# Performance work log

Hardware: AMD Instinct MI355X
Metric: run time of the kernel (lower is better)

## Reference

```python
import jax, jax.numpy as jnp
import numpy as np

N_NODES = 100000
N_EDGES = 1600000
K = 5  # TAGConv hops
F_IN, F_HID, F_OUT = 64, 128, 64


def setup_inputs() -> dict:
    key = jax.random.key(0)
    ks = jax.random.split(key, 6)
    x = jax.random.normal(ks[0], (N_NODES, F_IN), dtype=jnp.float32)
    edge_index = jax.random.randint(ks[1], (2, N_EDGES), 0, N_NODES, dtype=jnp.int32)
    edge_weight = jax.random.uniform(ks[2], (N_EDGES,), dtype=jnp.float32)
    # TAGConv layer l has (K+1) weight matrices stacked as [K+1, in, out] + one bias
    W0 = jax.random.normal(ks[3], (K + 1, F_IN, F_HID), dtype=jnp.float32) * 0.05
    b0 = jnp.zeros((F_HID,), dtype=jnp.float32)
    W1 = jax.random.normal(ks[4], (K + 1, F_HID, F_OUT), dtype=jnp.float32) * 0.05
    b1 = jnp.zeros((F_OUT,), dtype=jnp.float32)
    return {"x": x, "edge_index": edge_index, "edge_weight": edge_weight,
            "W0": W0, "b0": b0, "W1": W1, "b1": b1}


def _gcn_norm(edge_weight, row, col):
    # symmetric normalization, no added self-loops (TAGConv default with edge_weight)
    deg = jax.ops.segment_sum(edge_weight, col, num_segments=N_NODES)
    safe_deg = jnp.where(deg > 0, deg, 1.0)
    dis = jnp.where(deg > 0, jax.lax.rsqrt(safe_deg), 0.0)  # deg^-1/2, 0 for isolated
    return dis[row] * edge_weight * dis[col]


def _tag_conv(x, row, col, norm, W, b):
    # out = sum_{k=0..K} (A_norm^k x) @ W[k] + b
    out = x @ W[0]
    h = x
    for k in range(1, K + 1):
        msg = h[row] * norm[:, None]                    # gather + scale  [E, F]
        h = jax.ops.segment_sum(msg, col, num_segments=N_NODES)  # scatter-add [N, F]
        out = out + h @ W[k]
    return out + b


def reference(x, edge_index, edge_weight, W0, b0, W1, b1):
    row, col = edge_index[0], edge_index[1]
    norm = _gcn_norm(edge_weight, row, col)
    h = jax.nn.leaky_relu(_tag_conv(x, row, col, norm, W0, b0), negative_slope=0.01)
    h = jax.nn.leaky_relu(_tag_conv(h, row, col, norm, W1, b1), negative_slope=0.01)
    return h
```

## Files before the change

### kernel.cpp

```cpp
#include <hip/hip_runtime.h>


namespace {
constexpr int NN = 100000;
constexpr int NE = 1600000;
constexpr int TPB = 256;

typedef __attribute__((ext_vector_type(8))) short short8v;
typedef __attribute__((ext_vector_type(4))) float float4v;

__device__ __forceinline__ float bflo(unsigned p) { return __uint_as_float(p << 16); }
__device__ __forceinline__ float bfhi(unsigned p) { return __uint_as_float(p & 0xffff0000u); }
__device__ __forceinline__ unsigned f2bf(float x) {
  unsigned u = __float_as_uint(x);
  return (u + 0x7fffu + ((u >> 16) & 1u)) >> 16;
}
__device__ __forceinline__ unsigned pack2(float lo, float hi) {
  return f2bf(lo) | (f2bf(hi) << 16);
}

__global__ void pass1_kernel(const int* __restrict__ col, const float* __restrict__ w,
                             unsigned long long* __restrict__ acc64, int* __restrict__ rank) {
  int e = blockIdx.x * TPB + threadIdx.x;
  if (e >= NE) return;
  int c = col[e];
  unsigned long long v = (1ULL << 40) | (unsigned long long)__float2uint_rn(w[e] * 16777216.0f);
  unsigned long long old = atomicAdd(&acc64[c], v);
  rank[e] = (int)(old >> 40);
}

__global__ void dis_kernel(const unsigned long long* __restrict__ acc64,
                           float* __restrict__ dis) {
  int n = blockIdx.x * TPB + threadIdx.x;
  if (n >= NN) return;
  unsigned long long u = acc64[n] & ((1ULL << 40) - 1);
  float d = (float)u * (1.0f / 16777216.0f);
  dis[n] = d > 0.f ? rsqrtf(d) : 0.f;
}

__global__ void scan1_kernel(const unsigned long long* __restrict__ acc64,
                             int* __restrict__ excl, int* __restrict__ btot) {
  __shared__ int sh[1024];
  int i = blockIdx.x * 1024 + threadIdx.x;
  int v = (i < NN) ? (int)(acc64[i] >> 40) : 0;
  sh[threadIdx.x] = v;
  __syncthreads();
  for (int ofs = 1; ofs < 1024; ofs <<= 1) {
    int t = (threadIdx.x >= ofs) ? sh[threadIdx.x - ofs] : 0;
    __syncthreads();
    sh[threadIdx.x] += t;
    __syncthreads();
  }
  if (i < NN) excl[i] = sh[threadIdx.x] - v;
  if (threadIdx.x == 1023) btot[blockIdx.x] = sh[1023];
}

__global__ void scan2_kernel(int* __restrict__ btot, int nb) {
  __shared__ int sh[128];
  int t = threadIdx.x;
  if (t < nb) sh[t] = btot[t];
  __syncthreads();
  if (t == 0) {
    int run = 0;
    for (int b = 0; b < nb; ++b) { int x = sh[b]; sh[b] = run; run += x; }
  }
  __syncthreads();
  if (t < nb) btot[t] = sh[t];
}

__global__ void scan3_kernel(const int* __restrict__ excl, const int* __restrict__ btot,
                             int* __restrict__ rowptr) {
  int i = blockIdx.x * TPB + threadIdx.x;
  if (i < NN) rowptr[i] = excl[i] + btot[i >> 10];
  if (i == NN) rowptr[NN] = NE;
}

__global__ void fill2_kernel(const int* __restrict__ row, const int* __restrict__ col,
                             const float* __restrict__ w, const float* __restrict__ dis,
                             const int* __restrict__ rank, const int* __restrict__ rowptr,
                             int2* __restrict__ edges) {
  int e = blockIdx.x * TPB + threadIdx.x;
  if (e >= NE) return;
  int r = row[e], c = col[e];
  float nw = dis[r] * w[e] * dis[c];
  edges[rowptr[c] + rank[e]] = make_int2(r, __float_as_int(nw));
}

__global__ void wfrag0_kernel(const float* __restrict__ W0, short* __restrict__ F) {
  int t = blockIdx.x * TPB + threadIdx.x;
  if (t >= 12 * 8 * 64) return;
  int l = t & 63, nt = (t >> 6) & 7, s = t >> 9;
  int c = nt * 16 + (l & 15);
  int kb = s * 32 + (l >> 4) * 8;
  short8v v;
#pragma unroll
  for (int j = 0; j < 8; ++j) v[j] = (short)f2bf(W0[(kb + j) * 128 + c]);
  *(short8v*)(F + (size_t)t * 8) = v;
}

__global__ void wfrag1_kernel(const float* __restrict__ W1, short* __restrict__ F) {
  int t = blockIdx.x * TPB + threadIdx.x;
  if (t >= 4 * 24 * 64) return;
  int l = t & 63, nt = (t >> 6) % 24, s = t / (64 * 24);
  int J = nt * 16 + (l & 15);
  int fb = s * 32 + (l >> 4) * 8;
  const float* Wb = W1 + (size_t)(J >> 6) * (128 * 64) + (J & 63);
  short8v v;
#pragma unroll
  for (int j = 0; j < 8; ++j) v[j] = (short)f2bf(Wb[(size_t)(fb + j) * 64]);
  *(short8v*)(F + (size_t)t * 8) = v;
}

__global__ void convx_kernel(const float* __restrict__ x, unsigned* __restrict__ hcat) {
  unsigned idx = blockIdx.x * (unsigned)TPB + threadIdx.x;
  if (idx >= (unsigned)NN * 32u) return;
  unsigned n = idx >> 5, p = idx & 31u;
  float2 v = *(const float2*)(x + (size_t)n * 64 + p * 2);
  hcat[(size_t)n * 192 + p] = pack2(v.x, v.y);
}

__device__ __forceinline__ void fma8(float* a, uint4 p, float w) {
  a[0] = fmaf(bflo(p.x), w, a[0]); a[1] = fmaf(bfhi(p.x), w, a[1]);
  a[2] = fmaf(bflo(p.y), w, a[2]); a[3] = fmaf(bfhi(p.y), w, a[3]);
  a[4] = fmaf(bflo(p.z), w, a[4]); a[5] = fmaf(bfhi(p.z), w, a[5]);
  a[6] = fmaf(bflo(p.w), w, a[6]); a[7] = fmaf(bfhi(p.w), w, a[7]);
}

template <bool YADD, bool FINAL>
__global__ void hop_kernel(const unsigned short* __restrict__ src, int sstride,
                           const int2* __restrict__ edges, const int* __restrict__ rowptr,
                           const unsigned short* __restrict__ y,
                           unsigned short* __restrict__ dst, int dstride,
                           const float* __restrict__ bias, float* __restrict__ outf) {
  unsigned n = blockIdx.x * 32u + (threadIdx.x >> 3);
  unsigned lane = threadIdx.x & 7u;
  unsigned f0 = lane * 8u;
  int e = rowptr[n], e1 = rowptr[n + 1];
  float a[8] = {};
  for (; e + 1 < e1; e += 2) {
    int2 d0 = edges[e], d1 = edges[e + 1];
    uint4 p0 = *(const uint4*)(src + (size_t)(unsigned)d0.x * sstride + f0);
    uint4 p1 = *(const uint4*)(src + (size_t)(unsigned)d1.x * sstride + f0);
    fma8(a, p0, __int_as_float(d0.y));
    fma8(a, p1, __int_as_float(d1.y));
  }
  if (e < e1) {
    int2 d0 = edges[e];
    uint4 p0 = *(const uint4*)(src + (size_t)(unsigned)d0.x * sstride + f0);
    fma8(a, p0, __int_as_float(d0.y));
  }
  if (YADD) {
    uint4 yv = *(const uint4*)(y + (size_t)n * 384 + f0);
    a[0] += bflo(yv.x); a[1] += bfhi(yv.x);
    a[2] += bflo(yv.y); a[3] += bfhi(yv.y);
    a[4] += bflo(yv.z); a[5] += bfhi(yv.z);
    a[6] += bflo(yv.w); a[7] += bfhi(yv.w);
  }
  if (FINAL) {
    const float4* bp = (const float4*)(bias + f0);
    float4 bv0 = bp[0], bv1 = bp[1];
    float4 o0, o1;
    o0.x = a[0] + bv0.x; o0.y = a[1] + bv0.y; o0.z = a[2] + bv0.z; o0.w = a[3] + bv0.w;
    o1.x = a[4] + bv1.x; o1.y = a[5] + bv1.y; o1.z = a[6] + bv1.z; o1.w = a[7] + bv1.w;
    o0.x = o0.x >= 0.f ? o0.x : 0.01f * o0.x; o0.y = o0.y >= 0.f ? o0.y : 0.01f * o0.y;
    o0.z = o0.z >= 0.f ? o0.z : 0.01f * o0.z; o0.w = o0.w >= 0.f ? o0.w : 0.01f * o0.w;
    o1.x = o1.x >= 0.f ? o1.x : 0.01f * o1.x; o1.y = o1.y >= 0.f ? o1.y : 0.01f * o1.y;
    o1.z = o1.z >= 0.f ? o1.z : 0.01f * o1.z; o1.w = o1.w >= 0.f ? o1.w : 0.01f * o1.w;
    float4* op = (float4*)(outf + (size_t)n * 64 + f0);
    op[0] = o0; op[1] = o1;
  } else {
    uint4 st;
    st.x = pack2(a[0], a[1]); st.y = pack2(a[2], a[3]);
    st.z = pack2(a[4], a[5]); st.w = pack2(a[6], a[7]);
    *(uint4*)(dst + (size_t)n * dstride + f0) = st;
  }
}

__global__ void gemm_l0(const unsigned short* __restrict__ A, const short* __restrict__ W0f,
                        const float* __restrict__ bias, unsigned short* __restrict__ H1) {
  int wave = threadIdx.x >> 6, lane = threadIdx.x & 63;
  int lrow = lane & 15, lk = lane >> 4;
  unsigned r0 = blockIdx.x * 64u + (unsigned)wave * 16u;
  unsigned arow = r0 + (unsigned)lrow;
  if (arow >= NN) arow = NN - 1;
  const short8v* Ab = (const short8v*)(A + (size_t)arow * 384 + (unsigned)lk * 8);
  const short8v* Bb = (const short8v*)W0f + lane;
  float4v acc[8] = {};
#pragma unroll
  for (int s = 0; s < 12; ++s) {
    short8v a = Ab[s * 4];
#pragma unroll
    for (int nt = 0; nt < 8; ++nt) {
      short8v b = Bb[(s * 8 + nt) * 64];
      acc[nt] = __builtin_amdgcn_mfma_f32_16x16x32_bf16(a, b, acc[nt], 0, 0, 0);
    }
  }
#pragma unroll
  for (int nt = 0; nt < 8; ++nt) {
    int c = nt * 16 + lrow;
    float bv = bias[c];
#pragma unroll
    for (int r = 0; r < 4; ++r) {
      unsigned n = r0 + (unsigned)(lk * 4 + r);
      if (n < NN) {
        float v = acc[nt][r] + bv;
        v = v >= 0.f ? v : 0.01f * v;
        H1[(size_t)n * 128 + c] = (unsigned short)f2bf(v);
      }
    }
  }
}

__global__ void gemm_l1(const unsigned short* __restrict__ A, const short* __restrict__ W1f,
                        unsigned short* __restrict__ Y) {
  int wave = threadIdx.x >> 6, lane = threadIdx.x & 63;
  int lrow = lane & 15, lk = lane >> 4;
  unsigned r0 = blockIdx.x * 64u + (unsigned)wave * 16u;
  unsigned arow = r0 + (unsigned)lrow;
  if (arow >= NN) arow = NN - 1;
  const short8v* Ab = (const short8v*)(A + (size_t)arow * 128 + (unsigned)lk * 8);
  const short8v* Bb = (const short8v*)W1f + lane;
  float4v acc[24] = {};
#pragma unroll
  for (int s = 0; s < 4; ++s) {
    short8v a = Ab[s * 4];
#pragma unroll
    for (int nt = 0; nt < 24; ++nt) {
      short8v b = Bb[(s * 24 + nt) * 64];
      acc[nt] = __builtin_amdgcn_mfma_f32_16x16x32_bf16(a, b, acc[nt], 0, 0, 0);
    }
  }
#pragma unroll
  for (int nt = 0; nt < 24; ++nt) {
    int c = nt * 16 + lrow;
#pragma unroll
    for (int r = 0; r < 4; ++r) {
      unsigned n = r0 + (unsigned)(lk * 4 + r);
      if (n < NN) Y[(size_t)n * 384 + c] = (unsigned short)f2bf(acc[nt][r]);
    }
  }
}

}

extern "C" void kernel_launch(void* const* d_in, const int* in_sizes, int n_in,
                              void* d_out, int out_size, void* d_ws, size_t ws_size,
                              hipStream_t stream) {
  const float* x  = (const float*)d_in[0];
  const int*   ei = (const int*)d_in[1];
  const float* ew = (const float*)d_in[2];
  const float* W0 = (const float*)d_in[3];
  const float* b0 = (const float*)d_in[4];
  const float* W1 = (const float*)d_in[5];
  const float* b1 = (const float*)d_in[6];
  float* out = (float*)d_out;
  const int* row = ei;
  const int* col = ei + NE;

  constexpr size_t OFF_DIS    = 0;
  constexpr size_t OFF_ROWPTR = 100352;
  constexpr size_t OFF_BTOT   = OFF_ROWPTR + 100352;
  constexpr size_t OFF_EDGES  = OFF_BTOT + 128;
  constexpr size_t OFF_HCAT   = OFF_EDGES + 2 * (size_t)NE;
  constexpr size_t OFF_H1     = OFF_HCAT + (size_t)NN * 384 / 2;
  constexpr size_t WS_WORDS   = OFF_H1 + (size_t)NN * 128 / 2;
  if (ws_size < WS_WORDS * sizeof(float)) return;

  float* ws = (float*)d_ws;
  float* dis    = ws + OFF_DIS;
  int*   rowptr = (int*)(ws + OFF_ROWPTR);
  int*   btot   = (int*)(ws + OFF_BTOT);
  int2*  edges  = (int2*)(ws + OFF_EDGES);
  unsigned short* Hcat = (unsigned short*)(ws + OFF_HCAT);
  unsigned short* H1   = (unsigned short*)(ws + OFF_H1);
  short* W0f = (short*)(ws + OFF_DIS);
  short* W1f = (short*)(ws + OFF_DIS + 24576);
  unsigned long long* acc64 = (unsigned long long*)(ws + OFF_H1);
  int* excl = (int*)(ws + OFF_H1 + 200704);
  int* rank = (int*)Hcat;
  unsigned short* z0 = H1;
  unsigned short* z1 = H1 + (size_t)NN * 64;

  hipMemsetAsync(acc64, 0, NN * sizeof(unsigned long long), stream);
  pass1_kernel<<<(NE + TPB - 1) / TPB, TPB, 0, stream>>>(col, ew, acc64, rank);
  dis_kernel<<<(NN + TPB - 1) / TPB, TPB, 0, stream>>>(acc64, dis);
  scan1_kernel<<<98, 1024, 0, stream>>>(acc64, excl, btot);
  scan2_kernel<<<1, 128, 0, stream>>>(btot, 98);
  scan3_kernel<<<(NN + TPB) / TPB, TPB, 0, stream>>>(excl, btot, rowptr);
  fill2_kernel<<<(NE + TPB - 1) / TPB, TPB, 0, stream>>>(row, col, ew, dis, rank, rowptr, edges);
  wfrag0_kernel<<<24, TPB, 0, stream>>>(W0, W0f);
  wfrag1_kernel<<<24, TPB, 0, stream>>>(W1, W1f);

  convx_kernel<<<NN * 32 / TPB, TPB, 0, stream>>>(x, (unsigned*)Hcat);
  for (int k = 1; k <= 5; ++k) {
    hop_kernel<false, false><<<NN / 32, TPB, 0, stream>>>(
        Hcat + (k - 1) * 64, 384, edges, rowptr, nullptr,
        Hcat + k * 64, 384, nullptr, nullptr);
  }
  gemm_l0<<<(NN + 63) / 64, TPB, 0, stream>>>(Hcat, W0f, b0, H1);

  gemm_l1<<<(NN + 63) / 64, TPB, 0, stream>>>(H1, W1f, Hcat);
  const unsigned short* Y = Hcat;
  hop_kernel<true, false><<<NN / 32, TPB, 0, stream>>>(
      Y + 5 * 64, 384, edges, rowptr, Y + 4 * 64, z0, 64, nullptr, nullptr);
  hop_kernel<true, false><<<NN / 32, TPB, 0, stream>>>(
      z0, 64, edges, rowptr, Y + 3 * 64, z1, 64, nullptr, nullptr);
  hop_kernel<true, false><<<NN / 32, TPB, 0, stream>>>(
      z1, 64, edges, rowptr, Y + 2 * 64, z0, 64, nullptr, nullptr);
  hop_kernel<true, false><<<NN / 32, TPB, 0, stream>>>(
      z0, 64, edges, rowptr, Y + 1 * 64, z1, 64, nullptr, nullptr);
  hop_kernel<true, true><<<NN / 32, TPB, 0, stream>>>(
      z1, 64, edges, rowptr, Y + 0 * 64, nullptr, 0, b1, out);
}
```

Measured before the change: 656.8 us.

## Unroll hop gather by four, split gemm_l1 columns across grid, double pass1 work

The hop kernel's neighbor loop is unrolled from two to four edges per iteration so more independent gathers are in flight. gemm_l1 is split over a second grid dimension of three, so each block computes eight of the 24 output tiles. This cuts accumulator registers and raises occupancy, at the cost of reloading the A rows three times. pass1 now handles two edges per thread with half the blocks and no bounds check, which relies on NE dividing exactly by 512.

After: 620.8 us. -5.5%, faster.

```diff
diff --git a/kernel.cpp b/kernel.cpp
--- a/kernel.cpp
+++ b/kernel.cpp
@@ -21,12 +21,15 @@
 
 __global__ void pass1_kernel(const int* __restrict__ col, const float* __restrict__ w,
                              unsigned long long* __restrict__ acc64, int* __restrict__ rank) {
-  int e = blockIdx.x * TPB + threadIdx.x;
-  if (e >= NE) return;
-  int c = col[e];
-  unsigned long long v = (1ULL << 40) | (unsigned long long)__float2uint_rn(w[e] * 16777216.0f);
-  unsigned long long old = atomicAdd(&acc64[c], v);
-  rank[e] = (int)(old >> 40);
+  int e0 = blockIdx.x * (TPB * 2) + threadIdx.x;
+  int e1 = e0 + TPB;
+  int c0 = col[e0], c1 = col[e1];
+  unsigned long long v0 = (1ULL << 40) | (unsigned long long)__float2uint_rn(w[e0] * 16777216.0f);
+  unsigned long long v1 = (1ULL << 40) | (unsigned long long)__float2uint_rn(w[e1] * 16777216.0f);
+  unsigned long long o0 = atomicAdd(&acc64[c0], v0);
+  unsigned long long o1 = atomicAdd(&acc64[c1], v1);
+  rank[e0] = (int)(o0 >> 40);
+  rank[e1] = (int)(o1 >> 40);
 }
 
 __global__ void dis_kernel(const unsigned long long* __restrict__ acc64,
@@ -137,12 +140,24 @@
   unsigned f0 = lane * 8u;
   int e = rowptr[n], e1 = rowptr[n + 1];
   float a[8] = {};
-  for (; e + 1 < e1; e += 2) {
+  for (; e + 3 < e1; e += 4) {
+    int2 d0 = edges[e], d1 = edges[e + 1], d2 = edges[e + 2], d3 = edges[e + 3];
+    uint4 p0 = *(const uint4*)(src + (size_t)(unsigned)d0.x * sstride + f0);
+    uint4 p1 = *(const uint4*)(src + (size_t)(unsigned)d1.x * sstride + f0);
+    uint4 p2 = *(const uint4*)(src + (size_t)(unsigned)d2.x * sstride + f0);
+    uint4 p3 = *(const uint4*)(src + (size_t)(unsigned)d3.x * sstride + f0);
+    fma8(a, p0, __int_as_float(d0.y));
+    fma8(a, p1, __int_as_float(d1.y));
+    fma8(a, p2, __int_as_float(d2.y));
+    fma8(a, p3, __int_as_float(d3.y));
+  }
+  if (e + 1 < e1) {
     int2 d0 = edges[e], d1 = edges[e + 1];
     uint4 p0 = *(const uint4*)(src + (size_t)(unsigned)d0.x * sstride + f0);
     uint4 p1 = *(const uint4*)(src + (size_t)(unsigned)d1.x * sstride + f0);
     fma8(a, p0, __int_as_float(d0.y));
     fma8(a, p1, __int_as_float(d1.y));
+    e += 2;
   }
   if (e < e1) {
     int2 d0 = edges[e];
@@ -215,24 +230,25 @@
                         unsigned short* __restrict__ Y) {
   int wave = threadIdx.x >> 6, lane = threadIdx.x & 63;
   int lrow = lane & 15, lk = lane >> 4;
+  int yb = blockIdx.y * 8;
   unsigned r0 = blockIdx.x * 64u + (unsigned)wave * 16u;
   unsigned arow = r0 + (unsigned)lrow;
   if (arow >= NN) arow = NN - 1;
   const short8v* Ab = (const short8v*)(A + (size_t)arow * 128 + (unsigned)lk * 8);
   const short8v* Bb = (const short8v*)W1f + lane;
-  float4v acc[24] = {};
+  float4v acc[8] = {};
 #pragma unroll
   for (int s = 0; s < 4; ++s) {
     short8v a = Ab[s * 4];
 #pragma unroll
-    for (int nt = 0; nt < 24; ++nt) {
-      short8v b = Bb[(s * 24 + nt) * 64];
+    for (int nt = 0; nt < 8; ++nt) {
+      short8v b = Bb[(s * 24 + yb + nt) * 64];
       acc[nt] = __builtin_amdgcn_mfma_f32_16x16x32_bf16(a, b, acc[nt], 0, 0, 0);
     }
   }
 #pragma unroll
-  for (int nt = 0; nt < 24; ++nt) {
-    int c = nt * 16 + lrow;
+  for (int nt = 0; nt < 8; ++nt) {
+    int c = (yb + nt) * 16 + lrow;
 #pragma unroll
     for (int r = 0; r < 4; ++r) {
       unsigned n = r0 + (unsigned)(lk * 4 + r);
@@ -282,7 +298,7 @@
   unsigned short* z1 = H1 + (size_t)NN * 64;
 
   hipMemsetAsync(acc64, 0, NN * sizeof(unsigned long long), stream);
-  pass1_kernel<<<(NE + TPB - 1) / TPB, TPB, 0, stream>>>(col, ew, acc64, rank);
+  pass1_kernel<<<NE / (TPB * 2), TPB, 0, stream>>>(col, ew, acc64, rank);
   dis_kernel<<<(NN + TPB - 1) / TPB, TPB, 0, stream>>>(acc64, dis);
   scan1_kernel<<<98, 1024, 0, stream>>>(acc64, excl, btot);
   scan2_kernel<<<1, 128, 0, stream>>>(btot, 98);
@@ -299,7 +315,7 @@
   }
   gemm_l0<<<(NN + 63) / 64, TPB, 0, stream>>>(Hcat, W0f, b0, H1);
 
-  gemm_l1<<<(NN + 63) / 64, TPB, 0, stream>>>(H1, W1f, Hcat);
+  gemm_l1<<<dim3((NN + 63) / 64, 3), TPB, 0, stream>>>(H1, W1f, Hcat);
   const unsigned short* Y = Hcat;
   hop_kernel<true, false><<<NN / 32, TPB, 0, stream>>>(
       Y + 5 * 64, 384, edges, rowptr, Y + 4 * 64, z0, 64, nullptr, nullptr);
```
